# Performance work log

Measured on AMD Instinct MI355X. Metric: run time of the kernel, lower is better.

The kernel has to match this reference:

```python
import jax, jax.numpy as jnp
import numpy as np
from jax import lax

# ---- static graph layout: GPT-2-small-like full edge-pruning config ----
N_LAYERS, H = 12, 12
V_TOTAL = 2 + N_LAYERS * (H + 1)  # wte, wpe, then per layer: H attn outputs + 1 mlp

def _layer_dims(L):
    Vq = 2 + L * (H + 1)  # vertices visible to q/k/v at layer L (strictly upstream)
    Vm = Vq + H           # mlp additionally sees same-layer attn outputs
    return Vq, Vm

_LAYER_BASE = []
_p = 0
for _L in range(N_LAYERS):
    _LAYER_BASE.append(_p)
    _Vq, _Vm = _layer_dims(_L)
    _p += 3 * H * _Vq + _Vm  # q,k,v edges for all heads, then mlp edges
_LM_BASE = _p
P_TOTAL = _p + V_TOTAL       # lm_head reads every vertex


def _keep(Rch):
    """Given per-vertex reachability Rch (bz, V_TOTAL) bool, build the per-edge
    keep mask (bz, P_TOTAL): an edge survives iff its output vertex AND its
    input vertex are both reachable (== ~dangling in the torch code)."""
    bz = Rch.shape[0]
    parts = []
    for L in range(N_LAYERS):
        Vq, Vm = _layer_dims(L)
        a0 = 2 + L * (H + 1)
        ar = Rch[:, a0:a0 + H]        # (bz, H) attn_output-L-h reach
        mr = Rch[:, a0 + H]           # (bz,)  mlp-L reach
        kq = ar[:, None, :, None] & Rch[:, None, None, :Vq]  # (bz,3,H,Vq)
        parts.append(jnp.broadcast_to(kq, (bz, 3, H, Vq)).reshape(bz, 3 * H * Vq))
        parts.append(mr[:, None] & Rch[:, :Vm])
        del kq
    parts.append(Rch)                 # lm_head edges: keep iff input reachable
    return jnp.concatenate(parts, axis=1)


def _prune_dangling_edges(masks):
    bz = masks.shape[0]
    # --- forward reachability (reach-to-input), no-grad boolean sweep ---
    pos = masks > 0.0
    R = jnp.ones((bz, 2), bool)  # wte, wpe always reachable
    for L in range(N_LAYERS):
        Vq, Vm = _layer_dims(L)
        b = _LAYER_BASE[L]
        qkv = pos[:, b:b + 3 * H * Vq].reshape(bz, 3, H, Vq)
        # head reachable iff q AND k AND v each have >=1 live reachable input
        ar = jnp.all(jnp.any(qkv & R[:, None, None, :], axis=-1), axis=1)  # (bz,H)
        R = jnp.concatenate([R, ar], axis=1)                               # size Vm
        mm = pos[:, b + 3 * H * Vq: b + 3 * H * Vq + Vm]
        mr = jnp.any(mm & R, axis=-1)
        R = jnp.concatenate([R, mr[:, None]], axis=1)
    masks = jnp.where(_keep(R), masks, 0.0)
    # --- backward reachability (reach-to-output) on the pruned masks ---
    pos = masks > 0.0
    O = pos[:, _LM_BASE:]  # (bz, V_TOTAL): vertices fed into lm_head
    for L in range(N_LAYERS - 1, -1, -1):
        Vq, Vm = _layer_dims(L)
        b = _LAYER_BASE[L]
        a0 = 2 + L * (H + 1)
        # mlp first (it may make same-layer attn outputs output-reachable)
        mm = pos[:, b + 3 * H * Vq: b + 3 * H * Vq + Vm]
        O = O.at[:, :Vm].set(O[:, :Vm] | (mm & O[:, a0 + H][:, None]))
        qkv = pos[:, b:b + 3 * H * Vq].reshape(bz, 3, H, Vq)
        contrib = jnp.any(qkv & O[:, None, a0:a0 + H, None], axis=(1, 2))  # (bz,Vq)
        O = O.at[:, :Vq].set(O[:, :Vq] | contrib)
    masks = jnp.where(_keep(O), masks, 0.0)
    return masks


def setup_inputs() -> dict:
    key = jax.random.key(0)
    k1, k2 = jax.random.split(key)
    bz = 1024
    sample_params = jax.random.normal(k1, (P_TOTAL,), dtype=jnp.float32)
    unif = jax.random.uniform(k2, (bz, P_TOTAL), dtype=jnp.float32)
    return {"sample_params": sample_params, "unif": unif}


def reference(sample_params, unif):
    bz = unif.shape[0]
    prob = jnp.broadcast_to(jax.nn.sigmoid(sample_params)[None, :], unif.shape)
    window = lax.stop_gradient(prob * (1.0 - prob))  # detached window size
    prob = window * prob + (1.0 - window) * lax.stop_gradient(prob)
    masks = jnp.clip((prob - unif) / window + 0.5, 0.0, 1.0)
    masks = _prune_dangling_edges(masks)
    active = (masks > 0.001) & (masks < 1.0 - 0.001)
    n_samples = jnp.sum(active, axis=0).astype(masks.dtype)  # (P,)
    grad_wts = lax.stop_gradient(
        jnp.where(n_samples < 1.0, 0.0, bz / jnp.maximum(n_samples, 1.0)))
    masks = grad_wts * masks + (1.0 - grad_wts) * lax.stop_gradient(masks)
    return masks
```

## Files before the change

kernel.cpp:

```cpp
#include <hip/hip_runtime.h>
#include <stdint.h>

#define NL   12
#define PTOT 32936
#define LMB  32778
#define NCH  515
#define NCHP 520
#define NGRP 129
#define BMW  (NGRP * 4)
#define TPAD (NGRP * 256)
#define NSEG 445
#define TPB  512
#define NWV  (TPB / 64)

typedef float vf4 __attribute__((ext_vector_type(4)));

__device__ __constant__ int c_base[NL] = {0,86,653,1701,3230,5240,7731,10703,14156,18090,22505,27401};

__device__ __forceinline__ uint64_t ext(const uint64_t* P, uint32_t off) {
  uint32_t w = off >> 6, s = off & 63;
  uint64_t lo = P[w], hi = P[w + 1];
  return s ? ((lo >> s) | (hi << (64 - s))) : lo;
}

__device__ __forceinline__ uint64_t rbit(uint64_t r0, uint64_t r1, uint64_t r2, uint32_t idx) {
  uint64_t w = idx < 64 ? r0 : (idx < 128 ? r1 : r2);
  return (w >> (idx & 63)) & 1ull;
}

__device__ __forceinline__ uint64_t rext(uint64_t a0, uint64_t a1, uint64_t a2, uint32_t off) {
  uint32_t w = off >> 6, s = off & 63;
  uint64_t lo = (w == 0) ? a0 : ((w == 1) ? a1 : ((w == 2) ? a2 : 0ull));
  uint64_t hi = (w == 0) ? a1 : ((w == 1) ? a2 : 0ull);
  return s ? ((lo >> s) | (hi << (64 - s))) : lo;
}

__device__ __forceinline__ void orAt(uint64_t& r0, uint64_t& r1, uint64_t& r2,
                                     uint64_t val, uint32_t pos) {
  uint32_t w = pos >> 6, s = pos & 63;
  uint64_t lo = val << s;
  uint64_t hi = s ? (val >> (64 - s)) : 0ull;
  if (w == 0) { r0 |= lo; r1 |= hi; }
  else if (w == 1) { r1 |= lo; r2 |= hi; }
  else { r2 |= lo; }
}

__device__ __forceinline__ void maskLen(uint32_t len, uint64_t& m0, uint64_t& m1, uint64_t& m2) {
  m0 = (len >= 64) ? ~0ull : ((1ull << len) - 1ull);
  m1 = (len <= 64) ? 0ull : ((len >= 128) ? ~0ull : ((1ull << (len - 64)) - 1ull));
  m2 = (len <= 128) ? 0ull : ((1ull << (len - 128)) - 1ull);
}

__device__ __forceinline__ uint32_t ext12(uint64_t O0, uint64_t O1, uint64_t O2, uint32_t pos) {
  uint32_t w = pos >> 6, s = pos & 63;
  uint64_t lo = (w == 0) ? O0 : ((w == 1) ? O1 : O2);
  uint64_t hi = (w == 0) ? O1 : ((w == 1) ? O2 : 0ull);
  uint64_t v = s ? ((lo >> s) | (hi << (64 - s))) : lo;
  return (uint32_t)v & 0xFFFu;
}

__device__ __forceinline__ uint64_t spread4(uint64_t x) {
  x = (x | (x << 24)) & 0x000000FF000000FFull;
  x = (x | (x << 12)) & 0x000F000F000F000Full;
  x = (x | (x << 6))  & 0x0303030303030303ull;
  x = (x | (x << 3))  & 0x1111111111111111ull;
  return x;
}

__global__ void init_tables(const float* __restrict__ sp, float* __restrict__ pr,
                            float* __restrict__ wd) {
  int p = blockIdx.x * blockDim.x + threadIdx.x;
  if (p >= TPAD) return;
  if (p < PTOT) {
    float x = sp[p];
    float s = 1.0f / (1.0f + expf(-x));
    float w = __fmul_rn(s, __fsub_rn(1.0f, s));
    float pv = __fadd_rn(__fmul_rn(w, s), __fmul_rn(__fsub_rn(1.0f, w), s));
    pr[p] = pv; wd[p] = w;
  } else {
    pr[p] = 0.0f; wd[p] = 1.0f;
  }
}

__global__ __launch_bounds__(TPB) void fused_kernel(const float* __restrict__ unif,
                                                    const vf4* __restrict__ pr4,
                                                    const vf4* __restrict__ wd4,
                                                    float* __restrict__ out) {
  __shared__ uint64_t sPos[NCHP];
  __shared__ uint64_t sKeep[NCHP];
  __shared__ uint64_t sLv[4];
  __shared__ int sQn;
  __shared__ unsigned short sQ[NCH];

  const int tid  = threadIdx.x;
  const int lane = tid & 63;
  const int wv   = tid >> 6;
  const int row  = blockIdx.x;
  const vf4* up4 = (const vf4*)(unif + (size_t)row * PTOT);
  vf4*       op4 = (vf4*)(out + (size_t)row * PTOT);
  float*     op  = out + (size_t)row * PTOT;

  if (tid == 0) sQn = 0;

  {
    int G = wv;
    vf4 u = {0.f,0.f,0.f,0.f}, p = {0.f,0.f,0.f,0.f}, w = {1.f,1.f,1.f,1.f};
    bool inb = false;
    if (G < NGRP) {
      int e4 = G * 64 + lane;
      inb = e4 < (PTOT / 4);
      u = inb ? __builtin_nontemporal_load(&up4[e4]) : (vf4){0.f,0.f,0.f,0.f};
      p = pr4[e4]; w = wd4[e4];
    }
    while (G < NGRP) {
      const int Gn = G + NWV;
      vf4 un = {0.f,0.f,0.f,0.f}, pn = {0.f,0.f,0.f,0.f}, wn = {1.f,1.f,1.f,1.f};
      bool inbn = false;
      if (Gn < NGRP) {
        int e4n = Gn * 64 + lane;
        inbn = e4n < (PTOT / 4);
        un = inbn ? __builtin_nontemporal_load(&up4[e4n]) : (vf4){0.f,0.f,0.f,0.f};
        pn = pr4[e4n]; wn = wd4[e4n];
      }
      float m0 = __fadd_rn(__fdiv_rn(__fsub_rn(p.x, u.x), w.x), 0.5f);
      float m1 = __fadd_rn(__fdiv_rn(__fsub_rn(p.y, u.y), w.y), 0.5f);
      float m2 = __fadd_rn(__fdiv_rn(__fsub_rn(p.z, u.z), w.z), 0.5f);
      float m3 = __fadd_rn(__fdiv_rn(__fsub_rn(p.w, u.w), w.w), 0.5f);
      if (inb) {
        int e4 = G * 64 + lane;
        vf4 o;
        o.x = fminf(fmaxf(m0, 0.0f), 1.0f);
        o.y = fminf(fmaxf(m1, 0.0f), 1.0f);
        o.z = fminf(fmaxf(m2, 0.0f), 1.0f);
        o.w = fminf(fmaxf(m3, 0.0f), 1.0f);
        __builtin_nontemporal_store(o, &op4[e4]);
      }
      uint64_t b0 = __ballot(inb && (m0 > 0.0f));
      uint64_t b1 = __ballot(inb && (m1 > 0.0f));
      uint64_t b2 = __ballot(inb && (m2 > 0.0f));
      uint64_t b3 = __ballot(inb && (m3 > 0.0f));
      if (lane < 4) {
        uint64_t v = (lane == 0) ? b0 : (lane == 1) ? b1 : (lane == 2) ? b2 : b3;
        sKeep[G * 4 + lane] = v;
      }
      G = Gn; u = un; p = pn; w = wn; inb = inbn;
    }
  }
  __syncthreads();

  for (int G = tid; G < NGRP; G += TPB) {
    uint64_t b0 = sKeep[4 * G], b1 = sKeep[4 * G + 1];
    uint64_t b2 = sKeep[4 * G + 2], b3 = sKeep[4 * G + 3];
#pragma unroll
    for (int q = 0; q < 4; ++q) {
      uint64_t v = spread4((b0 >> (16 * q)) & 0xFFFFull)
                 | (spread4((b1 >> (16 * q)) & 0xFFFFull) << 1)
                 | (spread4((b2 >> (16 * q)) & 0xFFFFull) << 2)
                 | (spread4((b3 >> (16 * q)) & 0xFFFFull) << 3);
      sPos[4 * G + q] = v;
      sKeep[4 * G + q] = 0ull;
    }
  }
  for (int w = BMW + tid; w < NCHP; w += TPB) { sPos[w] = 0ull; sKeep[w] = 0ull; }
  __syncthreads();

  if (tid < 64) {
    uint64_t R0 = 3ull, R1 = 0ull, R2 = 0ull;
    const int g = lane;
#pragma unroll
    for (int L = 0; L < NL; ++L) {
      const int Vq = 2 + 13 * L;
      const int b  = c_base[L];
      bool pred = false;
      if (g < 36) {
        uint32_t off = (uint32_t)(b + g * Vq);
        uint64_t e0 = ext(sPos, off), e1 = ext(sPos, off + 64), e2 = ext(sPos, off + 128);
        pred = ((e0 & R0) | (e1 & R1) | (e2 & R2)) != 0ull;
      }
      uint64_t bal = __ballot(pred);
      uint64_t ar  = bal & (bal >> 12) & (bal >> 24) & 0xFFFull;
      orAt(R0, R1, R2, ar, (uint32_t)Vq);
      const int Vm = Vq + 12;
      uint32_t offm = (uint32_t)(b + 36 * Vq);
      uint64_t e0 = ext(sPos, offm), e1 = ext(sPos, offm + 64), e2 = ext(sPos, offm + 128);
      uint64_t mr = (((e0 & R0) | (e1 & R1) | (e2 & R2)) != 0ull) ? 1ull : 0ull;
      orAt(R0, R1, R2, mr, (uint32_t)Vm);
    }

    uint64_t O0 = ext(sPos, LMB)       & R0;
    uint64_t O1 = ext(sPos, LMB + 64)  & R1;
    uint64_t O2 = ext(sPos, LMB + 128) & ((1ull << 30) - 1ull) & R2;
    const int hg = g % 12;
#pragma unroll
    for (int L = NL - 1; L >= 0; --L) {
      const int Vq = 2 + 13 * L, Vm = Vq + 12;
      const int b  = c_base[L];
      if (rbit(O0, O1, O2, (uint32_t)Vm)) {
        uint64_t m0, m1, m2; maskLen((uint32_t)Vm, m0, m1, m2);
        uint32_t offm = (uint32_t)(b + 36 * Vq);
        O0 |= ext(sPos, offm)       & R0 & m0;
        O1 |= ext(sPos, offm + 64)  & R1 & m1;
        O2 |= ext(sPos, offm + 128) & R2 & m2;
      }
      uint32_t h12 = ext12(O0, O1, O2, (uint32_t)Vq);
      uint64_t q0, q1, q2; maskLen((uint32_t)Vq, q0, q1, q2);
      uint64_t c0 = 0ull, c1 = 0ull, c2 = 0ull;
      if (g < 36 && ((h12 >> hg) & 1u)) {
        uint32_t off = (uint32_t)(b + g * Vq);
        c0 = ext(sPos, off)       & R0 & q0;
        c1 = ext(sPos, off + 64)  & R1 & q1;
        c2 = ext(sPos, off + 128) & R2 & q2;
      }
#pragma unroll
      for (int d = 32; d; d >>= 1) {
        c0 |= __shfl_xor((unsigned long long)c0, d);
        c1 |= __shfl_xor((unsigned long long)c1, d);
        c2 |= __shfl_xor((unsigned long long)c2, d);
      }
      O0 |= c0; O1 |= c1; O2 |= c2;
    }
    if (lane == 0) {
      sLv[0] = R0 & O0; sLv[1] = R1 & O1; sLv[2] = R2 & O2; sLv[3] = 0ull;
    }
  }
  __syncthreads();

  {
    const uint64_t l0 = sLv[0], l1 = sLv[1], l2 = sLv[2];
    for (int s = tid; s < NSEG; s += TPB) {
      uint32_t p0, len;
      bool olive;
      if (s == NSEG - 1) {
        p0 = LMB; len = 158; olive = true;
      } else {
        int L = s / 37, j = s - L * 37;
        int Vq = 2 + 13 * L, b = c_base[L];
        if (j < 36) { p0 = (uint32_t)(b + j * Vq); len = (uint32_t)Vq;
                      olive = rbit(l0, l1, l2, (uint32_t)(Vq + (j % 12))) != 0ull; }
        else        { p0 = (uint32_t)(b + 36 * Vq); len = (uint32_t)(Vq + 12);
                      olive = rbit(l0, l1, l2, (uint32_t)(Vq + 12)) != 0ull; }
      }
      if (!olive) continue;
      uint32_t w0 = p0 >> 6, s0 = p0 & 63;
      uint64_t first = l0;
      if (len < 64) first &= (1ull << len) - 1ull;
      atomicOr((unsigned long long*)&sKeep[w0], (unsigned long long)(first << s0));
      uint32_t done = 64 - s0;
      uint32_t w = w0 + 1;
      while (done < len) {
        uint64_t v = rext(l0, l1, l2, done);
        uint32_t rem = len - done;
        if (rem < 64) v &= (1ull << rem) - 1ull;
        atomicOr((unsigned long long*)&sKeep[w], (unsigned long long)v);
        done += 64; ++w;
      }
    }
  }
  __syncthreads();

  for (int w = tid; w < NCH; w += TPB) {
    uint64_t pm = sPos[w];
    if (!pm) continue;
    uint64_t z = pm & ~sKeep[w];
    if (z) {
      sPos[w] = z;
      int k = atomicAdd(&sQn, 1);
      sQ[k] = (unsigned short)w;
    }
  }
  __syncthreads();
  {
    const int qn = sQn;
    for (int k = wv; k < qn; k += NWV) {
      int w = sQ[k];
      uint64_t z = sPos[w];
      if ((z >> lane) & 1ull) op[w * 64 + lane] = 0.0f;
    }
  }
}

extern "C" void kernel_launch(void* const* d_in, const int* in_sizes, int n_in,
                              void* d_out, int out_size, void* d_ws, size_t ws_size,
                              hipStream_t stream) {
  const float* sp   = (const float*)d_in[0];
  const float* unif = (const float*)d_in[1];
  float* out = (float*)d_out;
  char* ws = (char*)d_ws;
  float* pr = (float*)ws;
  float* wd = (float*)(ws + 132096);
  int bz = in_sizes[1] / PTOT;

  init_tables<<<dim3(TPAD / 256), dim3(256), 0, stream>>>(sp, pr, wd);
  fused_kernel<<<dim3(bz), dim3(TPB), 0, stream>>>(
      unif, (const vf4*)pr, (const vf4*)wd, out);
}
```

Baseline: 304.1 us.

## Defer mask output write until keep bits are known, recomputing values in a final pass

Measured after the change: 269.6 us. 11.3% less time.

```diff
diff --git a/kernel.cpp b/kernel.cpp
--- a/kernel.cpp
+++ b/kernel.cpp
@@ -89,8 +89,6 @@
   __shared__ uint64_t sPos[NCHP];
   __shared__ uint64_t sKeep[NCHP];
   __shared__ uint64_t sLv[4];
-  __shared__ int sQn;
-  __shared__ unsigned short sQ[NCH];
 
   const int tid  = threadIdx.x;
   const int lane = tid & 63;
@@ -98,9 +96,6 @@
   const int row  = blockIdx.x;
   const vf4* up4 = (const vf4*)(unif + (size_t)row * PTOT);
   vf4*       op4 = (vf4*)(out + (size_t)row * PTOT);
-  float*     op  = out + (size_t)row * PTOT;
-
-  if (tid == 0) sQn = 0;
 
   {
     int G = wv;
@@ -109,7 +104,7 @@
     if (G < NGRP) {
       int e4 = G * 64 + lane;
       inb = e4 < (PTOT / 4);
-      u = inb ? __builtin_nontemporal_load(&up4[e4]) : (vf4){0.f,0.f,0.f,0.f};
+      u = inb ? up4[e4] : (vf4){0.f,0.f,0.f,0.f};
       p = pr4[e4]; w = wd4[e4];
     }
     while (G < NGRP) {
@@ -119,22 +114,13 @@
       if (Gn < NGRP) {
         int e4n = Gn * 64 + lane;
         inbn = e4n < (PTOT / 4);
-        un = inbn ? __builtin_nontemporal_load(&up4[e4n]) : (vf4){0.f,0.f,0.f,0.f};
+        un = inbn ? up4[e4n] : (vf4){0.f,0.f,0.f,0.f};
         pn = pr4[e4n]; wn = wd4[e4n];
       }
       float m0 = __fadd_rn(__fdiv_rn(__fsub_rn(p.x, u.x), w.x), 0.5f);
       float m1 = __fadd_rn(__fdiv_rn(__fsub_rn(p.y, u.y), w.y), 0.5f);
       float m2 = __fadd_rn(__fdiv_rn(__fsub_rn(p.z, u.z), w.z), 0.5f);
       float m3 = __fadd_rn(__fdiv_rn(__fsub_rn(p.w, u.w), w.w), 0.5f);
-      if (inb) {
-        int e4 = G * 64 + lane;
-        vf4 o;
-        o.x = fminf(fmaxf(m0, 0.0f), 1.0f);
-        o.y = fminf(fmaxf(m1, 0.0f), 1.0f);
-        o.z = fminf(fmaxf(m2, 0.0f), 1.0f);
-        o.w = fminf(fmaxf(m3, 0.0f), 1.0f);
-        __builtin_nontemporal_store(o, &op4[e4]);
-      }
       uint64_t b0 = __ballot(inb && (m0 > 0.0f));
       uint64_t b1 = __ballot(inb && (m1 > 0.0f));
       uint64_t b2 = __ballot(inb && (m2 > 0.0f));
@@ -258,23 +244,28 @@
   }
   __syncthreads();
 
-  for (int w = tid; w < NCH; w += TPB) {
-    uint64_t pm = sPos[w];
-    if (!pm) continue;
-    uint64_t z = pm & ~sKeep[w];
-    if (z) {
-      sPos[w] = z;
-      int k = atomicAdd(&sQn, 1);
-      sQ[k] = (unsigned short)w;
-    }
-  }
-  __syncthreads();
   {
-    const int qn = sQn;
-    for (int k = wv; k < qn; k += NWV) {
-      int w = sQ[k];
-      uint64_t z = sPos[w];
-      if ((z >> lane) & 1ull) op[w * 64 + lane] = 0.0f;
+    const int sh = 4 * (lane & 15);
+    const int kw0 = lane >> 4;
+    for (int G = wv; G < NGRP; G += NWV) {
+      int e4 = G * 64 + lane;
+      bool inb = e4 < (PTOT / 4);
+      vf4 u = inb ? up4[e4] : (vf4){0.f,0.f,0.f,0.f};
+      vf4 p = pr4[e4];
+      vf4 w = wd4[e4];
+      uint32_t k = (uint32_t)(sKeep[G * 4 + kw0] >> sh) & 0xFu;
+      float m0 = __fadd_rn(__fdiv_rn(__fsub_rn(p.x, u.x), w.x), 0.5f);
+      float m1 = __fadd_rn(__fdiv_rn(__fsub_rn(p.y, u.y), w.y), 0.5f);
+      float m2 = __fadd_rn(__fdiv_rn(__fsub_rn(p.z, u.z), w.z), 0.5f);
+      float m3 = __fadd_rn(__fdiv_rn(__fsub_rn(p.w, u.w), w.w), 0.5f);
+      if (inb) {
+        vf4 o;
+        o.x = (k & 1u) ? fminf(fmaxf(m0, 0.0f), 1.0f) : 0.0f;
+        o.y = (k & 2u) ? fminf(fmaxf(m1, 0.0f), 1.0f) : 0.0f;
+        o.z = (k & 4u) ? fminf(fmaxf(m2, 0.0f), 1.0f) : 0.0f;
+        o.w = (k & 8u) ? fminf(fmaxf(m3, 0.0f), 1.0f) : 0.0f;
+        __builtin_nontemporal_store(o, &op4[e4]);
+      }
     }
   }
 }
```
